# Kernel tuning notes

Hardware: AMD Instinct MI355X
Metric: run time of the kernel (lower is better)

Reference implementation:

```python
import jax, jax.numpy as jnp
import numpy as np

B, T, D, H = 2, 2048, 1024, 16


def setup_inputs() -> dict:
    key = jax.random.key(0)
    kx, kq, kk, kv, ko = jax.random.split(key, 5)
    s = D ** -0.5  # linear-layer init scale
    return {
        "x": jax.random.normal(kx, (B, T, D), dtype=jnp.float32),
        "Wq": jax.random.normal(kq, (D, D), dtype=jnp.float32) * s,
        "Wk": jax.random.normal(kk, (D, D), dtype=jnp.float32) * s,
        "Wv": jax.random.normal(kv, (D, D), dtype=jnp.float32) * s,
        "Wo": jax.random.normal(ko, (D, D), dtype=jnp.float32) * s,
        "quadrant_weights": jnp.array([1.0, -0.5, -0.5, 0.25], dtype=jnp.float32),
    }


def reference(x, Wq, Wk, Wv, Wo, quadrant_weights):
    Bx, Tx, Dx = x.shape
    d = Dx // H          # head dim
    h = d // 2           # quadrant (half-head) dim
    scale = h ** -0.5

    # projections -> (B, H, T, d)
    q = (x @ Wq).reshape(Bx, Tx, H, d).transpose(0, 2, 1, 3)
    k = (x @ Wk).reshape(Bx, Tx, H, d).transpose(0, 2, 1, 3)
    v = (x @ Wv).reshape(Bx, Tx, H, d).transpose(0, 2, 1, 3)

    q1, q2 = q[..., :h], q[..., h:]
    k1, k2 = k[..., :h], k[..., h:]

    w = jax.nn.softmax(quadrant_weights)
    # Fused quadrant sum: w0*q1k1^T + w1*q1k2^T + w2*q2k1^T + w3*q2k2^T
    # == q1 @ (w0*k1 + w1*k2)^T + q2 @ (w2*k1 + w3*k2)^T  (same math, fewer matmuls)
    k_eff1 = w[0] * k1 + w[1] * k2
    k_eff2 = w[2] * k1 + w[3] * k2
    attn = (jnp.einsum('bhqc,bhkc->bhqk', q1, k_eff1)
            + jnp.einsum('bhqc,bhkc->bhqk', q2, k_eff2)) * scale
    attn = jax.nn.softmax(attn, axis=-1)

    out = jnp.einsum('bhqk,bhkd->bhqd', attn, v)
    out = out.transpose(0, 2, 1, 3).reshape(Bx, Tx, Dx)
    return out @ Wo
```

## Files before the change

### kernel.cpp

```cpp
#include <hip/hip_runtime.h>

typedef unsigned short u16;
typedef unsigned int u32;
typedef __attribute__((ext_vector_type(8))) short short8;
typedef __attribute__((ext_vector_type(4))) short short4v;
typedef __attribute__((ext_vector_type(4))) float f32x4;
typedef __attribute__((ext_vector_type(16))) float f32x16;
typedef __attribute__((ext_vector_type(2))) unsigned u32x2;
typedef __attribute__((ext_vector_type(4))) unsigned u32x4;

__device__ __forceinline__ u16 f2bf(float f) {
  union { float f; unsigned u; } a; a.f = f;
  unsigned u = a.u + 0x7fffu + ((a.u >> 16) & 1u);
  return (u16)(u >> 16);
}
__device__ __forceinline__ float bf2f(short s) {
  union { unsigned u; float f; } a; a.u = ((unsigned)(unsigned short)s) << 16;
  return a.f;
}
__device__ __forceinline__ u32 cvtpk(float lo, float hi_) {
  u32 r; asm("v_cvt_pk_bf16_f32 %0, %1, %2" : "=v"(r) : "v"(lo), "v"(hi_)); return r;
}
__device__ __forceinline__ void plswap(u32 &x, u32 &y) {
  asm("v_permlane32_swap_b32 %0, %1" : "+v"(x), "+v"(y));
}
__device__ __forceinline__ short8 as_short8(u32x4 v) {
  union { u32x4 u; short8 s; } c; c.u = v; return c.s;
}
__device__ __forceinline__ float fexp2(float x) {
  float r; asm("v_exp_f32 %0, %1" : "=v"(r) : "v"(x)); return r;
}
__device__ __forceinline__ void gload16(const u16* g, u16* l) {
  __builtin_amdgcn_global_load_lds(
      (__attribute__((address_space(1))) void*)(u16*)g,
      (__attribute__((address_space(3))) void*)l, 16, 0, 0);
}
__device__ __forceinline__ void keep8(short8 v) {
  union { short8 s; int i[4]; } u; u.s = v;
  asm volatile("" :: "v"(u.i[0]), "v"(u.i[1]), "v"(u.i[2]), "v"(u.i[3]));
}
__device__ __forceinline__ void wait_vm4() { asm volatile("s_waitcnt vmcnt(4)" ::: "memory"); }
__device__ __forceinline__ void wait_vm3() { asm volatile("s_waitcnt vmcnt(3)" ::: "memory"); }
__device__ __forceinline__ void wait_vm0() { asm volatile("s_waitcnt vmcnt(0)" ::: "memory"); }
__device__ __forceinline__ void barrier_raw() {
  __builtin_amdgcn_sched_barrier(0);
  __builtin_amdgcn_s_barrier();
  __builtin_amdgcn_sched_barrier(0);
}

__global__ void cvt_x_kernel(const float* __restrict__ x, u16* __restrict__ xb) {
  int i = (blockIdx.x * 256 + threadIdx.x) * 8;
  float4 a = *(const float4*)(x + i);
  float4 b = *(const float4*)(x + i + 4);
  short8 v;
  v[0] = (short)f2bf(a.x); v[1] = (short)f2bf(a.y);
  v[2] = (short)f2bf(a.z); v[3] = (short)f2bf(a.w);
  v[4] = (short)f2bf(b.x); v[5] = (short)f2bf(b.y);
  v[6] = (short)f2bf(b.z); v[7] = (short)f2bf(b.w);
  *(short8*)(xb + i) = v;
}

__global__ void prep_w_kernel(const float* __restrict__ Wq, const float* __restrict__ Wk,
                              const float* __restrict__ Wv, const float* __restrict__ Wo,
                              const float* __restrict__ qw,
                              u16* __restrict__ Wcat, u16* __restrict__ Wot) {
  __shared__ float tile[32][33];
  const int z = blockIdx.z;
  const int n0 = blockIdx.x * 32, k0 = blockIdx.y * 32;
  const float* src = (z == 0) ? Wq : (z == 1) ? Wk : (z == 2) ? Wv : Wo;
  float w0 = 0.f, w1 = 0.f, w2 = 0.f, w3 = 0.f;
  if (z == 1) {
    float a = qw[0], b = qw[1], c = qw[2], d = qw[3];
    float mx = fmaxf(fmaxf(a, b), fmaxf(c, d));
    float ea = expf(a - mx), eb = expf(b - mx), ec = expf(c - mx), ed = expf(d - mx);
    float s = ea + eb + ec + ed;
    w0 = ea / s; w1 = eb / s; w2 = ec / s; w3 = ed / s;
  }
  #pragma unroll
  for (int i = 0; i < 32; i += 8) {
    int k = k0 + threadIdx.y + i;
    int n = n0 + threadIdx.x;
    float v;
    if (z == 1) {
      int c = n & 63;
      if (c < 32) v = w0 * src[k * 1024 + n]      + w1 * src[k * 1024 + n + 32];
      else        v = w2 * src[k * 1024 + n - 32] + w3 * src[k * 1024 + n];
    } else {
      v = src[k * 1024 + n];
    }
    tile[threadIdx.y + i][threadIdx.x] = v;
  }
  __syncthreads();
  #pragma unroll
  for (int i = 0; i < 32; i += 8) {
    int n = n0 + threadIdx.y + i;
    int k = k0 + threadIdx.x;
    u16 v = f2bf(tile[threadIdx.x][threadIdx.y + i]);
    if (z < 3) Wcat[(size_t)(z * 1024 + n) * 1024 + k] = v;
    else       Wot[(size_t)n * 1024 + k] = v;
  }
}

template<int MODE, int BM>
__global__ __launch_bounds__(256, 2)
void gemm_k(const u16* __restrict__ A, const u16* __restrict__ Bm,
            u16* __restrict__ out_q, u16* __restrict__ out_k,
            u16* __restrict__ out_vt, float* __restrict__ out_f) {
  constexpr int WM = BM / 2;
  constexpr int MR = WM / 16;
  constexpr int RW = BM / 4;
  constexpr int NST = BM / 64 + 2;
  __shared__ u16 At[3][BM * 32];
  __shared__ u16 Bt[3][128 * 32];
  const int tid = threadIdx.x;
  const int wid = tid >> 6, lane = tid & 63;
  const int l15 = lane & 15, l4 = lane >> 4;

  const int nwg = gridDim.x * gridDim.y;
  const int cpx = nwg >> 3;
  int bid = blockIdx.y * gridDim.x + blockIdx.x;
  int wg = (bid & 7) * cpx + (bid >> 3);
  const int bx = wg % gridDim.x, by = wg / gridDim.x;
  const int mblk = by * BM, nblk = bx * 128;
  const int wm = (wid >> 1) * WM, wn = (wid & 1) * 64;
  f32x4 acc[MR][4] = {};

  const int rr = lane >> 2;
  const int cA = (lane & 3) * 8;
  const u16* gB = Bm + (size_t)(nblk + wid * 32 + rr) * 1024 + cA;
  const u16* gA = A + (size_t)(mblk + wid * RW + rr) * 1024 + cA;

  auto STAGE = [&](int ib, int kt) {
    #pragma unroll
    for (int q = 0; q < RW / 16; ++q)
      gload16(gA + (size_t)q * 16 * 1024 + kt, &At[ib][(wid * RW + q * 16) * 32]);
    #pragma unroll
    for (int q = 0; q < 2; ++q)
      gload16(gB + (size_t)q * 16 * 1024 + kt, &Bt[ib][(wid * 32 + q * 16) * 32]);
  };

  STAGE(0, 0);
  STAGE(1, 32);
  int ib = 0, ibw = 2;
  for (int s = 0; s < 32; ++s) {
    if (s < 31) {
      if constexpr (NST == 4) wait_vm4();
      else wait_vm3();
    } else wait_vm0();
    barrier_raw();
    if (s + 2 < 32) STAGE(ibw, (s + 2) * 32);
    short8 af[MR], bf[4];
    #pragma unroll
    for (int i = 0; i < MR; ++i)
      af[i] = *(const short8*)(&At[ib][(wm + i * 16 + l15) * 32 + l4 * 8]);
    #pragma unroll
    for (int j = 0; j < 4; ++j)
      bf[j] = *(const short8*)(&Bt[ib][(wn + j * 16 + l15) * 32 + l4 * 8]);
    #pragma unroll
    for (int i = 0; i < MR; ++i)
      #pragma unroll
      for (int j = 0; j < 4; ++j)
        acc[i][j] = __builtin_amdgcn_mfma_f32_16x16x32_bf16(af[i], bf[j], acc[i][j], 0, 0, 0);
    ib = (ib == 2) ? 0 : ib + 1;
    ibw = (ibw == 2) ? 0 : ibw + 1;
  }

  const float QSCALE = 0.17677669529663687f * 1.4426950408889634f;
  #pragma unroll
  for (int i = 0; i < MR; ++i) {
    int m_g = mblk + wm + i * 16 + l4 * 4;
    #pragma unroll
    for (int j = 0; j < 4; ++j) {
      int n_g = nblk + wn + j * 16 + l15;
      f32x4 v = acc[i][j];
      if (MODE == 1) {
        #pragma unroll
        for (int jj = 0; jj < 4; ++jj)
          out_f[(size_t)(m_g + jj) * 1024 + n_g] = v[jj];
      } else {
        if (n_g < 2048) {
          u16* dst; float sc;
          if (n_g < 1024) { dst = out_q; sc = QSCALE; } else { dst = out_k; sc = 1.0f; }
          int nn = n_g & 1023;
          #pragma unroll
          for (int jj = 0; jj < 4; ++jj)
            dst[(size_t)(m_g + jj) * 1024 + nn] = f2bf(v[jj] * sc);
        } else {
          int c = n_g - 2048;
          int b = m_g >> 11, t = m_g & 2047;
          short4v p;
          p[0] = (short)f2bf(v[0]); p[1] = (short)f2bf(v[1]);
          p[2] = (short)f2bf(v[2]); p[3] = (short)f2bf(v[3]);
          *(short4v*)(out_vt + ((size_t)((b << 4) + (c >> 6)) * 64 + (c & 63)) * 2048 + t) = p;
        }
      }
    }
  }
}

__global__ __launch_bounds__(256, 4)
void attn_k(const u16* __restrict__ Q, const u16* __restrict__ Kb,
            const u16* __restrict__ Vt, u16* __restrict__ Opart,
            float* __restrict__ L) {
  __shared__ u16 lk[2][64 * 64];
  __shared__ u16 lv[2][64 * 64];
  const int tid = threadIdx.x, wid = tid >> 6, lane = tid & 63;
  const int l31 = lane & 31, hi = lane >> 5;

  int bid = blockIdx.y * 16 + blockIdx.x;
  int wg = (bid & 7) * 128 + (bid >> 3);
  const int qt = wg & 15;
  const int yy = wg >> 4;
  const int half = yy & 1, bh = yy >> 1;
  const int b = bh >> 4, h = bh & 15;
  const int qrow = qt * 128 + wid * 32 + l31;

  short8 qf[4];
  #pragma unroll
  for (int cs = 0; cs < 4; ++cs)
    qf[cs] = *(const short8*)(Q + (size_t)(b * 2048 + qrow) * 1024 + h * 64 + cs * 16 + hi * 8);
  #pragma unroll
  for (int cs = 0; cs < 4; ++cs) keep8(qf[cs]);

  const int sr = lane >> 3;
  const int sc8 = (lane & 7) ^ sr;
  const u16* Kg = Kb + ((size_t)b * 2048 + half * 1024) * 1024 + h * 64 + sc8 * 8;
  const u16* Vg = Vt + (size_t)bh * 64 * 2048 + half * 1024 + sc8 * 8;
  const int s0i = wid * 2;
  const int swz = l31 & 7;

  short8 onesf;
  #pragma unroll
  for (int j = 0; j < 8; ++j) onesf[j] = (short)0x3F80;
  const f32x16 z16 = {};

  f32x16 accO0 = {}, accO1 = {}, sacc = {};

  auto STAGE = [&](int tt, int ibx) {
    #pragma unroll
    for (int s2 = 0; s2 < 2; ++s2) {
      int s = s0i + s2;
      int r = s * 8 + sr;
      gload16(Kg + (size_t)(tt * 64 + r) * 1024, &lk[ibx][s * 512]);
      gload16(Vg + (size_t)r * 2048 + tt * 64, &lv[ibx][s * 512]);
    }
  };

  STAGE(0, 0);

  for (int t = 0; t < 16; ++t) {
    wait_vm0();
    barrier_raw();
    if (t + 1 < 16) STAGE(t + 1, (t + 1) & 1);

    const u16* kb = lk[t & 1];
    const u16* vb = lv[t & 1];

    f32x16 s0v, s1v;
    __builtin_amdgcn_s_setprio(1);
    {
      short8 k0 = *(const short8*)(kb + l31 * 64 + ((hi ^ swz) * 8));
      short8 k1 = *(const short8*)(kb + (32 + l31) * 64 + ((hi ^ swz) * 8));
      s0v = __builtin_amdgcn_mfma_f32_32x32x16_bf16(k0, qf[0], z16, 0, 0, 0);
      s1v = __builtin_amdgcn_mfma_f32_32x32x16_bf16(k1, qf[0], z16, 0, 0, 0);
    }
    #pragma unroll
    for (int cs = 1; cs < 4; ++cs) {
      int ch = cs * 2 + hi;
      short8 k0 = *(const short8*)(kb + l31 * 64 + ((ch ^ swz) * 8));
      short8 k1 = *(const short8*)(kb + (32 + l31) * 64 + ((ch ^ swz) * 8));
      s0v = __builtin_amdgcn_mfma_f32_32x32x16_bf16(k0, qf[cs], s0v, 0, 0, 0);
      s1v = __builtin_amdgcn_mfma_f32_32x32x16_bf16(k1, qf[cs], s1v, 0, 0, 0);
    }
    __builtin_amdgcn_s_setprio(0);

    #pragma unroll
    for (int i = 0; i < 16; ++i) { s0v[i] = fexp2(s0v[i]); s1v[i] = fexp2(s1v[i]); }

    short8 paS[4];
    #pragma unroll
    for (int hf = 0; hf < 2; ++hf) {
      #pragma unroll
      for (int kq = 0; kq < 2; ++kq) {
        float p0, p1, p2, p3, p4, p5, p6, p7;
        if (hf == 0) {
          p0 = s0v[kq*8+0]; p1 = s0v[kq*8+1]; p2 = s0v[kq*8+2]; p3 = s0v[kq*8+3];
          p4 = s0v[kq*8+4]; p5 = s0v[kq*8+5]; p6 = s0v[kq*8+6]; p7 = s0v[kq*8+7];
        } else {
          p0 = s1v[kq*8+0]; p1 = s1v[kq*8+1]; p2 = s1v[kq*8+2]; p3 = s1v[kq*8+3];
          p4 = s1v[kq*8+4]; p5 = s1v[kq*8+5]; p6 = s1v[kq*8+6]; p7 = s1v[kq*8+7];
        }
        u32 A = cvtpk(p0, p1), B = cvtpk(p2, p3);
        u32 C = cvtpk(p4, p5), D = cvtpk(p6, p7);
        plswap(A, C);
        plswap(B, D);
        u32x4 w; w[0] = A; w[1] = B; w[2] = C; w[3] = D;
        paS[hf * 2 + kq] = as_short8(w);
      }
    }

    __builtin_amdgcn_s_setprio(1);
    #pragma unroll
    for (int ks = 0; ks < 4; ++ks) {
      int ch = ks * 2 + hi;
      short8 v0 = *(const short8*)(vb + l31 * 64 + ((ch ^ swz) * 8));
      short8 v1 = *(const short8*)(vb + (32 + l31) * 64 + ((ch ^ swz) * 8));
      accO0 = __builtin_amdgcn_mfma_f32_32x32x16_bf16(v0, paS[ks], accO0, 0, 0, 0);
      accO1 = __builtin_amdgcn_mfma_f32_32x32x16_bf16(v1, paS[ks], accO1, 0, 0, 0);
      sacc  = __builtin_amdgcn_mfma_f32_32x32x16_bf16(onesf, paS[ks], sacc, 0, 0, 0);
    }
    __builtin_amdgcn_s_setprio(0);
  }

  u16* Po = Opart + (size_t)(half * 4096 + b * 2048 + qrow) * 1024 + h * 64;
  #pragma unroll
  for (int g = 0; g < 4; ++g) {
    u32x2 pr;
    pr[0] = cvtpk(accO0[4*g],    accO0[4*g+1]);
    pr[1] = cvtpk(accO0[4*g+2],  accO0[4*g+3]);
    *(u32x2*)(Po + 8*g + 4*hi) = pr;
    u32x2 pr2;
    pr2[0] = cvtpk(accO1[4*g],   accO1[4*g+1]);
    pr2[1] = cvtpk(accO1[4*g+2], accO1[4*g+3]);
    *(u32x2*)(Po + 32 + 8*g + 4*hi) = pr2;
  }
  if (hi == 0)
    L[(size_t)(half * 32 + bh) * 2048 + qrow] = sacc[0];
}

__global__ __launch_bounds__(256)
void merge_k(const u16* __restrict__ Opart, const float* __restrict__ L,
             u16* __restrict__ Ob) {
  int i = blockIdx.x * 256 + threadIdx.x;
  int e = i * 8;
  int row = e >> 10;
  int col = e & 1023;
  int h = col >> 6;
  int b = row >> 11;
  int tr = row & 2047;
  int bh = b * 16 + h;
  float l1 = L[(size_t)bh * 2048 + tr];
  float l2 = L[(size_t)(32 + bh) * 2048 + tr];
  float inv = 1.0f / (l1 + l2);
  short8 o1 = *(const short8*)(Opart + (size_t)row * 1024 + col);
  short8 o2 = *(const short8*)(Opart + (size_t)(4096 + row) * 1024 + col);
  u32x4 w;
  #pragma unroll
  for (int j = 0; j < 4; ++j) {
    float lo = (bf2f(o1[2*j])   + bf2f(o2[2*j]))   * inv;
    float hi_ = (bf2f(o1[2*j+1]) + bf2f(o2[2*j+1])) * inv;
    w[j] = cvtpk(lo, hi_);
  }
  *(u32x4*)(Ob + (size_t)row * 1024 + col) = w;
}

extern "C" void kernel_launch(void* const* d_in, const int* in_sizes, int n_in,
                              void* d_out, int out_size, void* d_ws, size_t ws_size,
                              hipStream_t stream) {
  const float* x  = (const float*)d_in[0];
  const float* Wq = (const float*)d_in[1];
  const float* Wk = (const float*)d_in[2];
  const float* Wv = (const float*)d_in[3];
  const float* Wo = (const float*)d_in[4];
  const float* qw = (const float*)d_in[5];

  char* w = (char*)d_ws;
  u16* Wot   = (u16*)(w);
  u16* Qb    = (u16*)(w + (2u  << 20));
  u16* Kb    = (u16*)(w + (10u << 20));
  u16* Vtb   = (u16*)(w + (18u << 20));
  u16* xb    = (u16*)(w + (26u << 20));
  u16* Wcat  = (u16*)(w + (34u << 20));
  u16* Opart = (u16*)(w + (26u << 20));
  float* L   = (float*)(w + (42u << 20));
  u16* Ob    = Qb;

  cvt_x_kernel<<<2048, 256, 0, stream>>>(x, xb);
  prep_w_kernel<<<dim3(32, 32, 4), dim3(32, 8), 0, stream>>>(Wq, Wk, Wv, Wo, qw, Wcat, Wot);
  gemm_k<0, 128><<<dim3(24, 32), 256, 0, stream>>>(xb, Wcat, Qb, Kb, Vtb, nullptr);
  attn_k<<<dim3(16, 64), 256, 0, stream>>>(Qb, Kb, Vtb, Opart, L);
  merge_k<<<2048, 256, 0, stream>>>(Opart, L, Ob);
  gemm_k<1, 64><<<dim3(8, 64), 256, 0, stream>>>(Ob, Wot, nullptr, nullptr, nullptr, (float*)d_out);
}
```

Baseline: 122.0 us.

## Fuse split-KV merge into output projection GEMM and merge prep kernels

Removes the separate merge kernel by having the output projection GEMM load both partial attention outputs through registers, combine them with the inverse of the summed softmax denominators held in shared memory, and write the result into the LDS A tile. This saves a full write and read of the merged activation and one launch. The x conversion and weight prep kernels are merged into a single launch. The trade-off is that A-tile loading goes through registers and VALU work instead of direct global-to-LDS loads, and the wait counts and pipeline depth change, which could stall the GEMM main loop.

After: 137.7 us. +12.9%, slower.

```diff
diff --git a/kernel.cpp b/kernel.cpp
--- a/kernel.cpp
+++ b/kernel.cpp
@@ -39,34 +39,42 @@
   union { short8 s; int i[4]; } u; u.s = v;
   asm volatile("" :: "v"(u.i[0]), "v"(u.i[1]), "v"(u.i[2]), "v"(u.i[3]));
 }
+__device__ __forceinline__ void wait_vm6() { asm volatile("s_waitcnt vmcnt(6)" ::: "memory"); }
 __device__ __forceinline__ void wait_vm4() { asm volatile("s_waitcnt vmcnt(4)" ::: "memory"); }
-__device__ __forceinline__ void wait_vm3() { asm volatile("s_waitcnt vmcnt(3)" ::: "memory"); }
+__device__ __forceinline__ void wait_vm2() { asm volatile("s_waitcnt vmcnt(2)" ::: "memory"); }
 __device__ __forceinline__ void wait_vm0() { asm volatile("s_waitcnt vmcnt(0)" ::: "memory"); }
+__device__ __forceinline__ void wait_lgkm0() { asm volatile("s_waitcnt lgkmcnt(0)" ::: "memory"); }
 __device__ __forceinline__ void barrier_raw() {
   __builtin_amdgcn_sched_barrier(0);
   __builtin_amdgcn_s_barrier();
   __builtin_amdgcn_sched_barrier(0);
 }
 
-__global__ void cvt_x_kernel(const float* __restrict__ x, u16* __restrict__ xb) {
-  int i = (blockIdx.x * 256 + threadIdx.x) * 8;
-  float4 a = *(const float4*)(x + i);
-  float4 b = *(const float4*)(x + i + 4);
-  short8 v;
-  v[0] = (short)f2bf(a.x); v[1] = (short)f2bf(a.y);
-  v[2] = (short)f2bf(a.z); v[3] = (short)f2bf(a.w);
-  v[4] = (short)f2bf(b.x); v[5] = (short)f2bf(b.y);
-  v[6] = (short)f2bf(b.z); v[7] = (short)f2bf(b.w);
-  *(short8*)(xb + i) = v;
-}
-
-__global__ void prep_w_kernel(const float* __restrict__ Wq, const float* __restrict__ Wk,
-                              const float* __restrict__ Wv, const float* __restrict__ Wo,
-                              const float* __restrict__ qw,
-                              u16* __restrict__ Wcat, u16* __restrict__ Wot) {
+__global__ void cvtprep_kernel(const float* __restrict__ x, u16* __restrict__ xb,
+                               const float* __restrict__ Wq, const float* __restrict__ Wk,
+                               const float* __restrict__ Wv, const float* __restrict__ Wo,
+                               const float* __restrict__ qw,
+                               u16* __restrict__ Wcat, u16* __restrict__ Wot) {
   __shared__ float tile[32][33];
-  const int z = blockIdx.z;
-  const int n0 = blockIdx.x * 32, k0 = blockIdx.y * 32;
+  const int blk = blockIdx.x;
+  const int tid = threadIdx.x;
+  if (blk < 2048) {
+    int i = (blk * 256 + tid) * 8;
+    float4 a = *(const float4*)(x + i);
+    float4 b = *(const float4*)(x + i + 4);
+    short8 v;
+    v[0] = (short)f2bf(a.x); v[1] = (short)f2bf(a.y);
+    v[2] = (short)f2bf(a.z); v[3] = (short)f2bf(a.w);
+    v[4] = (short)f2bf(b.x); v[5] = (short)f2bf(b.y);
+    v[6] = (short)f2bf(b.z); v[7] = (short)f2bf(b.w);
+    *(short8*)(xb + i) = v;
+    return;
+  }
+  const int pb = blk - 2048;
+  const int z = pb >> 10;
+  const int xy = pb & 1023;
+  const int n0 = (xy & 31) * 32, k0 = (xy >> 5) * 32;
+  const int tx = tid & 31, ty = tid >> 5;
   const float* src = (z == 0) ? Wq : (z == 1) ? Wk : (z == 2) ? Wv : Wo;
   float w0 = 0.f, w1 = 0.f, w2 = 0.f, w3 = 0.f;
   if (z == 1) {
@@ -78,8 +86,8 @@
   }
   #pragma unroll
   for (int i = 0; i < 32; i += 8) {
-    int k = k0 + threadIdx.y + i;
-    int n = n0 + threadIdx.x;
+    int k = k0 + ty + i;
+    int n = n0 + tx;
     float v;
     if (z == 1) {
       int c = n & 63;
@@ -88,28 +96,27 @@
     } else {
       v = src[k * 1024 + n];
     }
-    tile[threadIdx.y + i][threadIdx.x] = v;
+    tile[ty + i][tx] = v;
   }
   __syncthreads();
   #pragma unroll
   for (int i = 0; i < 32; i += 8) {
-    int n = n0 + threadIdx.y + i;
-    int k = k0 + threadIdx.x;
-    u16 v = f2bf(tile[threadIdx.x][threadIdx.y + i]);
+    int n = n0 + ty + i;
+    int k = k0 + tx;
+    u16 v = f2bf(tile[tx][ty + i]);
     if (z < 3) Wcat[(size_t)(z * 1024 + n) * 1024 + k] = v;
     else       Wot[(size_t)n * 1024 + k] = v;
   }
 }
 
-template<int MODE, int BM>
+template<int BM>
 __global__ __launch_bounds__(256, 2)
 void gemm_k(const u16* __restrict__ A, const u16* __restrict__ Bm,
             u16* __restrict__ out_q, u16* __restrict__ out_k,
-            u16* __restrict__ out_vt, float* __restrict__ out_f) {
+            u16* __restrict__ out_vt) {
   constexpr int WM = BM / 2;
   constexpr int MR = WM / 16;
   constexpr int RW = BM / 4;
-  constexpr int NST = BM / 64 + 2;
   __shared__ u16 At[3][BM * 32];
   __shared__ u16 Bt[3][128 * 32];
   const int tid = threadIdx.x;
@@ -143,10 +150,7 @@
   STAGE(1, 32);
   int ib = 0, ibw = 2;
   for (int s = 0; s < 32; ++s) {
-    if (s < 31) {
-      if constexpr (NST == 4) wait_vm4();
-      else wait_vm3();
-    } else wait_vm0();
+    if (s < 31) wait_vm4(); else wait_vm0();
     barrier_raw();
     if (s + 2 < 32) STAGE(ibw, (s + 2) * 32);
     short8 af[MR], bf[4];
@@ -173,26 +177,20 @@
     for (int j = 0; j < 4; ++j) {
       int n_g = nblk + wn + j * 16 + l15;
       f32x4 v = acc[i][j];
-      if (MODE == 1) {
+      if (n_g < 2048) {
+        u16* dst; float sc;
+        if (n_g < 1024) { dst = out_q; sc = QSCALE; } else { dst = out_k; sc = 1.0f; }
+        int nn = n_g & 1023;
         #pragma unroll
         for (int jj = 0; jj < 4; ++jj)
-          out_f[(size_t)(m_g + jj) * 1024 + n_g] = v[jj];
+          dst[(size_t)(m_g + jj) * 1024 + nn] = f2bf(v[jj] * sc);
       } else {
-        if (n_g < 2048) {
-          u16* dst; float sc;
-          if (n_g < 1024) { dst = out_q; sc = QSCALE; } else { dst = out_k; sc = 1.0f; }
-          int nn = n_g & 1023;
-          #pragma unroll
-          for (int jj = 0; jj < 4; ++jj)
-            dst[(size_t)(m_g + jj) * 1024 + nn] = f2bf(v[jj] * sc);
-        } else {
-          int c = n_g - 2048;
-          int b = m_g >> 11, t = m_g & 2047;
-          short4v p;
-          p[0] = (short)f2bf(v[0]); p[1] = (short)f2bf(v[1]);
-          p[2] = (short)f2bf(v[2]); p[3] = (short)f2bf(v[3]);
-          *(short4v*)(out_vt + ((size_t)((b << 4) + (c >> 6)) * 64 + (c & 63)) * 2048 + t) = p;
-        }
+        int c = n_g - 2048;
+        int b = m_g >> 11, t = m_g & 2047;
+        short4v p;
+        p[0] = (short)f2bf(v[0]); p[1] = (short)f2bf(v[1]);
+        p[2] = (short)f2bf(v[2]); p[3] = (short)f2bf(v[3]);
+        *(short4v*)(out_vt + ((size_t)((b << 4) + (c >> 6)) * 64 + (c & 63)) * 2048 + t) = p;
       }
     }
   }
@@ -328,30 +326,116 @@
     L[(size_t)(half * 32 + bh) * 2048 + qrow] = sacc[0];
 }
 
-__global__ __launch_bounds__(256)
-void merge_k(const u16* __restrict__ Opart, const float* __restrict__ L,
-             u16* __restrict__ Ob) {
-  int i = blockIdx.x * 256 + threadIdx.x;
-  int e = i * 8;
-  int row = e >> 10;
-  int col = e & 1023;
-  int h = col >> 6;
-  int b = row >> 11;
-  int tr = row & 2047;
-  int bh = b * 16 + h;
-  float l1 = L[(size_t)bh * 2048 + tr];
-  float l2 = L[(size_t)(32 + bh) * 2048 + tr];
-  float inv = 1.0f / (l1 + l2);
-  short8 o1 = *(const short8*)(Opart + (size_t)row * 1024 + col);
-  short8 o2 = *(const short8*)(Opart + (size_t)(4096 + row) * 1024 + col);
-  u32x4 w;
-  #pragma unroll
-  for (int j = 0; j < 4; ++j) {
-    float lo = (bf2f(o1[2*j])   + bf2f(o2[2*j]))   * inv;
-    float hi_ = (bf2f(o1[2*j+1]) + bf2f(o2[2*j+1])) * inv;
-    w[j] = cvtpk(lo, hi_);
-  }
-  *(u32x4*)(Ob + (size_t)row * 1024 + col) = w;
+__global__ __launch_bounds__(256, 2)
+void gemm1_fused(const u16* __restrict__ Op, const float* __restrict__ L,
+                 const u16* __restrict__ Bm, float* __restrict__ out_f) {
+  constexpr int BM = 64;
+  constexpr int MR = 2;
+  __shared__ u16 At[3][BM * 32];
+  __shared__ u16 Bt[3][128 * 32];
+  __shared__ float Linv[16 * 64];
+  const int tid = threadIdx.x;
+  const int wid = tid >> 6, lane = tid & 63;
+  const int l15 = lane & 15, l4 = lane >> 4;
+
+  const int nwg = gridDim.x * gridDim.y;
+  const int cpx = nwg >> 3;
+  int bid = blockIdx.y * gridDim.x + blockIdx.x;
+  int wg = (bid & 7) * cpx + (bid >> 3);
+  const int bx = wg % gridDim.x, by = wg / gridDim.x;
+  const int mblk = by * BM, nblk = bx * 128;
+  const int wm = (wid >> 1) * 32, wn = (wid & 1) * 64;
+  f32x4 acc[MR][4] = {};
+
+  {
+    int h = tid >> 4;
+    int r0 = (tid & 15) * 4;
+    int m0 = mblk + r0;
+    int b0 = m0 >> 11, tr0 = m0 & 2047;
+    int bh = b0 * 16 + h;
+    float4 l1 = *(const float4*)(L + (size_t)bh * 2048 + tr0);
+    float4 l2 = *(const float4*)(L + (size_t)(32 + bh) * 2048 + tr0);
+    float4 iv;
+    iv.x = 1.0f / (l1.x + l2.x); iv.y = 1.0f / (l1.y + l2.y);
+    iv.z = 1.0f / (l1.z + l2.z); iv.w = 1.0f / (l1.w + l2.w);
+    *(float4*)(&Linv[h * 64 + r0]) = iv;
+  }
+  wait_lgkm0();
+  barrier_raw();
+
+  const int rr = lane >> 2;
+  const int cA = (lane & 3) * 8;
+  const int lrow = wid * 16 + rr;
+  const u16* gA1 = Op + (size_t)(mblk + lrow) * 1024 + cA;
+  const u16* gA2 = gA1 + (size_t)4096 * 1024;
+  const u16* gB = Bm + (size_t)(nblk + wid * 32 + rr) * 1024 + cA;
+
+  u32x4 rA1[2], rA2[2];
+
+  auto LOADA = [&](int set, int kt) {
+    rA1[set] = *(const u32x4*)(gA1 + kt);
+    rA2[set] = *(const u32x4*)(gA2 + kt);
+  };
+  auto STAGEB = [&](int ib, int kt) {
+    #pragma unroll
+    for (int q = 0; q < 2; ++q)
+      gload16(gB + (size_t)q * 16 * 1024 + kt, &Bt[ib][(wid * 32 + q * 16) * 32]);
+  };
+  auto WRITEA = [&](int set, int ib, int tile) {
+    float inv = Linv[(tile >> 1) * 64 + lrow];
+    union { u32x4 u; short8 s; } a1, a2;
+    a1.u = rA1[set]; a2.u = rA2[set];
+    u32x4 w;
+    #pragma unroll
+    for (int j = 0; j < 4; ++j)
+      w[j] = cvtpk((bf2f(a1.s[2*j])   + bf2f(a2.s[2*j]))   * inv,
+                   (bf2f(a1.s[2*j+1]) + bf2f(a2.s[2*j+1])) * inv);
+    *(u32x4*)(&At[ib][lrow * 32 + cA]) = w;
+  };
+
+  LOADA(0, 0);
+  STAGEB(0, 0);
+  LOADA(1, 32);
+  STAGEB(1, 32);
+  wait_vm6();
+  WRITEA(0, 0, 0);
+
+  for (int s = 0; s < 32; ++s) {
+    if (s < 30) wait_vm2(); else wait_vm0();
+    wait_lgkm0();
+    barrier_raw();
+    if (s + 1 < 32) WRITEA((s + 1) & 1, (s + 1) % 3, s + 1);
+    if (s + 2 < 32) {
+      LOADA(s & 1, (s + 2) * 32);
+      STAGEB((s + 2) % 3, (s + 2) * 32);
+    }
+    const int ib = s % 3;
+    short8 af[MR], bf[4];
+    #pragma unroll
+    for (int i = 0; i < MR; ++i)
+      af[i] = *(const short8*)(&At[ib][(wm + i * 16 + l15) * 32 + l4 * 8]);
+    #pragma unroll
+    for (int j = 0; j < 4; ++j)
+      bf[j] = *(const short8*)(&Bt[ib][(wn + j * 16 + l15) * 32 + l4 * 8]);
+    #pragma unroll
+    for (int i = 0; i < MR; ++i)
+      #pragma unroll
+      for (int j = 0; j < 4; ++j)
+        acc[i][j] = __builtin_amdgcn_mfma_f32_16x16x32_bf16(af[i], bf[j], acc[i][j], 0, 0, 0);
+  }
+
+  #pragma unroll
+  for (int i = 0; i < MR; ++i) {
+    int m_g = mblk + wm + i * 16 + l4 * 4;
+    #pragma unroll
+    for (int j = 0; j < 4; ++j) {
+      int n_g = nblk + wn + j * 16 + l15;
+      f32x4 v = acc[i][j];
+      #pragma unroll
+      for (int jj = 0; jj < 4; ++jj)
+        out_f[(size_t)(m_g + jj) * 1024 + n_g] = v[jj];
+    }
+  }
 }
 
 extern "C" void kernel_launch(void* const* d_in, const int* in_sizes, int n_in,
@@ -373,12 +457,9 @@
   u16* Wcat  = (u16*)(w + (34u << 20));
   u16* Opart = (u16*)(w + (26u << 20));
   float* L   = (float*)(w + (42u << 20));
-  u16* Ob    = Qb;
-
-  cvt_x_kernel<<<2048, 256, 0, stream>>>(x, xb);
-  prep_w_kernel<<<dim3(32, 32, 4), dim3(32, 8), 0, stream>>>(Wq, Wk, Wv, Wo, qw, Wcat, Wot);
-  gemm_k<0, 128><<<dim3(24, 32), 256, 0, stream>>>(xb, Wcat, Qb, Kb, Vtb, nullptr);
+
+  cvtprep_kernel<<<6144, 256, 0, stream>>>(x, xb, Wq, Wk, Wv, Wo, qw, Wcat, Wot);
+  gemm_k<128><<<dim3(24, 32), 256, 0, stream>>>(xb, Wcat, Qb, Kb, Vtb);
   attn_k<<<dim3(16, 64), 256, 0, stream>>>(Qb, Kb, Vtb, Opart, L);
-  merge_k<<<2048, 256, 0, stream>>>(Opart, L, Ob);
-  gemm_k<1, 64><<<dim3(8, 64), 256, 0, stream>>>(Ob, Wot, nullptr, nullptr, nullptr, (float*)d_out);
-}
+  gemm1_fused<<<dim3(8, 64), 256, 0, stream>>>(Opart, L, Wot, (float*)d_out);
+}
```
